# Kernel tuning notes

Hardware: AMD Instinct MI355X
Metric: run time of the kernel (lower is better)

Reference implementation:

```python
import jax, jax.numpy as jnp
import numpy as np

BLANK_IDX = -1  # resolves to V-1
BATCH_FIRST = False
IS_PROBS = False


def setup_inputs() -> dict:
    key = jax.random.key(0)
    k1, k2 = jax.random.split(key)
    T, N, V = 2048, 32, 1024
    logits = jax.random.normal(k1, (T, N, V), dtype=jnp.float32)
    in_lens = jax.random.randint(k2, (N,), 1, T + 1).astype(jnp.int64)
    return {"logits": logits, "in_lens": in_lens}


def reference(logits, in_lens):
    # logits: (T, N, V) since batch_first=False
    V = logits.shape[2]
    blank = (BLANK_IDX + V) % V  # = V - 1
    logp = jax.nn.log_softmax(logits, axis=2)
    x = jnp.transpose(logp, (1, 0, 2))  # (N, T, V)
    max_ = jnp.max(x, axis=2)            # (N, T)
    argmax = jnp.argmax(x, axis=2)       # (N, T)
    N, T = argmax.shape

    keep = argmax != blank
    dedup = jnp.concatenate(
        [keep[:, :1], keep[:, 1:] & (argmax[:, 1:] != argmax[:, :-1])], axis=1
    )
    in_len_mask = jnp.arange(T)[None, :] < in_lens[:, None]  # (N, T)
    keep = dedup & in_len_mask
    max_ = jnp.where(in_len_mask, max_, 0.0)

    out_lens = keep.sum(axis=1)  # (N,)
    # stream compaction: position of each kept token within its row
    pos = jnp.cumsum(keep, axis=1) - 1               # (N, T)
    safe_pos = jnp.where(keep, pos, T)               # out-of-bounds -> dropped
    rows = jnp.broadcast_to(jnp.arange(N)[:, None], (N, T))
    # torch masked_scatter_ semantics: overwrite first out_lens[n] slots,
    # leave remaining entries as original argmax values ("undefined" region)
    paths = argmax.at[rows, safe_pos].set(argmax, mode="drop")

    max_total = max_.sum(axis=1)  # (N,)
    if not BATCH_FIRST:
        paths = paths.T  # (T, N)
    return max_total, paths, out_lens
```

## Files before the change

### kernel.cpp

```cpp
#include <hip/hip_runtime.h>
#include <hip/hip_bf16.h>


#define WAVE 64

typedef float nvec4 __attribute__((ext_vector_type(4)));

template <int CH>
__global__ __launch_bounds__(256) void row_lse_kernel(
    const float* __restrict__ logits,
    float* __restrict__ rmaxT, int* __restrict__ rargT,
    float* __restrict__ out_paths,
    int T, int N, int rows) {
  const int lane = threadIdx.x & (WAVE - 1);
  const int w    = threadIdx.x >> 6;
  const int row  = blockIdx.x * 4 + w;
  const bool active = row < rows;
  const int V = CH * 256;
  const float* p = logits + (size_t)(active ? row : 0) * V;
  const nvec4* p4 = (const nvec4*)p;

  float m = -3.4e38f;
  int   mi = 0;
  nvec4 v[CH];
#pragma unroll
  for (int c = 0; c < CH; ++c) {
    v[c] = __builtin_nontemporal_load(p4 + c * 64 + lane);
    const int idx = c * 256 + lane * 4;
    if (v[c].x > m) { m = v[c].x; mi = idx; }
    if (v[c].y > m) { m = v[c].y; mi = idx + 1; }
    if (v[c].z > m) { m = v[c].z; mi = idx + 2; }
    if (v[c].w > m) { m = v[c].w; mi = idx + 3; }
  }
#pragma unroll
  for (int off = 32; off; off >>= 1) {
    const float om = __shfl_down(m, off);
    const int   oi = __shfl_down(mi, off);
    if (om > m || (om == m && oi < mi)) { m = om; mi = oi; }
  }
  m = __shfl(m, 0);

  float s = 0.f;
#pragma unroll
  for (int c = 0; c < CH; ++c)
    s += __expf(v[c].x - m) + __expf(v[c].y - m) +
         __expf(v[c].z - m) + __expf(v[c].w - m);
#pragma unroll
  for (int off = 32; off; off >>= 1) s += __shfl_down(s, off);

  __shared__ float s_path[4];
  if (lane == 0 && active) {
    const int t = row / N, n = row % N;
    rmaxT[(size_t)n * T + t] = -__logf(s);
    rargT[(size_t)n * T + t] = mi;
    s_path[w] = (float)mi;
  }
  __syncthreads();
  if (threadIdx.x < 4) {
    const int r = blockIdx.x * 4 + threadIdx.x;
    if (r < rows) out_paths[r] = s_path[threadIdx.x];
  }
}

__global__ __launch_bounds__(256) void row_lse_generic(
    const float* __restrict__ logits,
    float* __restrict__ rmaxT, int* __restrict__ rargT,
    float* __restrict__ out_paths,
    int T, int N, int V, int rows) {
  const int lane = threadIdx.x & (WAVE - 1);
  const int w    = threadIdx.x >> 6;
  const int row  = blockIdx.x * 4 + w;
  const bool active = row < rows;
  const float* p = logits + (size_t)(active ? row : 0) * V;

  float m = -3.4e38f; int mi = 0;
  for (int i = lane; i < V; i += WAVE) {
    const float x = p[i];
    if (x > m) { m = x; mi = i; }
  }
  for (int off = 32; off; off >>= 1) {
    const float om = __shfl_down(m, off);
    const int   oi = __shfl_down(mi, off);
    if (om > m || (om == m && oi < mi)) { m = om; mi = oi; }
  }
  m = __shfl(m, 0);
  float s = 0.f;
  for (int i = lane; i < V; i += WAVE) s += __expf(p[i] - m);
  for (int off = 32; off; off >>= 1) s += __shfl_down(s, off);

  __shared__ float s_path[4];
  if (lane == 0 && active) {
    const int t = row / N, n = row % N;
    rmaxT[(size_t)n * T + t] = -__logf(s);
    rargT[(size_t)n * T + t] = mi;
    s_path[w] = (float)mi;
  }
  __syncthreads();
  if (threadIdx.x < 4) {
    const int r = blockIdx.x * 4 + threadIdx.x;
    if (r < rows) out_paths[r] = s_path[threadIdx.x];
  }
}

#define CB 256
__global__ __launch_bounds__(CB) void ctc_compact_kernel(
    const float* __restrict__ rmaxT, const int* __restrict__ rargT,
    const int* __restrict__ in_lens, float* __restrict__ out,
    int T, int N, int V) {
  const int n = blockIdx.x;
  const int tid = threadIdx.x;
  const int L = in_lens[n];
  const int blank = V - 1;
  const int items = (T + CB - 1) / CB;
  const int t0 = tid * items;

  float* out_total = out;
  float* out_paths = out + N;
  float* out_lens  = out + N + (size_t)T * N;

  const float* rm = rmaxT + (size_t)n * T;
  const int*   ra = rargT + (size_t)n * T;

  int   cnt = 0;
  float sum = 0.f;
  int prev = (t0 > 0 && t0 <= T) ? ra[t0 - 1] : -1;
  for (int i = 0; i < items; ++i) {
    const int t = t0 + i;
    if (t >= T) break;
    const int a = ra[t];
    const bool keep = (t < L) && (a != blank) && (t == 0 || a != prev);
    prev = a;
    cnt += keep ? 1 : 0;
    if (t < L) sum += rm[t];
  }

  __shared__ int   s_cnt[CB];
  __shared__ float s_sum[CB];
  s_cnt[tid] = cnt;
  s_sum[tid] = sum;
  __syncthreads();
  for (int off = 1; off < CB; off <<= 1) {
    const int   c  = (tid >= off) ? s_cnt[tid - off] : 0;
    const float sv = (tid >= off) ? s_sum[tid - off] : 0.f;
    __syncthreads();
    s_cnt[tid] += c;
    s_sum[tid] += sv;
    __syncthreads();
  }
  const int prefix = s_cnt[tid] - cnt;
  if (tid == 0) {
    out_total[n] = s_sum[CB - 1];
    out_lens[n]  = (float)s_cnt[CB - 1];
  }

  int pos = prefix;
  prev = (t0 > 0 && t0 <= T) ? ra[t0 - 1] : -1;
  for (int i = 0; i < items; ++i) {
    const int t = t0 + i;
    if (t >= T) break;
    const int a = ra[t];
    const bool keep = (t < L) && (a != blank) && (t == 0 || a != prev);
    prev = a;
    if (keep) {
      out_paths[(size_t)pos * N + n] = (float)a;
      ++pos;
    }
  }
}

extern "C" void kernel_launch(void* const* d_in, const int* in_sizes, int n_in,
                              void* d_out, int out_size, void* d_ws, size_t ws_size,
                              hipStream_t stream) {
  const float* logits = (const float*)d_in[0];
  const int* in_lens  = (const int*)d_in[1];
  float* out = (float*)d_out;

  const int N = in_sizes[1];
  const int T = (out_size - 2 * N) / N;
  const long long total = in_sizes[0];
  const int V = (int)(total / ((long long)T * N));
  const int rows = T * N;

  float* rmaxT = (float*)d_ws;
  int*   rargT = (int*)((char*)d_ws + (size_t)rows * sizeof(float));
  float* out_paths = out + N;

  const int grid1 = (rows + 3) / 4;

  if (V == 1024) {
    row_lse_kernel<4><<<grid1, 256, 0, stream>>>(logits, rmaxT, rargT, out_paths, T, N, rows);
  } else if (V == 512) {
    row_lse_kernel<2><<<grid1, 256, 0, stream>>>(logits, rmaxT, rargT, out_paths, T, N, rows);
  } else if (V == 2048) {
    row_lse_kernel<8><<<grid1, 256, 0, stream>>>(logits, rmaxT, rargT, out_paths, T, N, rows);
  } else {
    row_lse_generic<<<grid1, 256, 0, stream>>>(logits, rmaxT, rargT, out_paths, T, N, V, rows);
  }

  ctc_compact_kernel<<<N, CB, 0, stream>>>(rmaxT, rargT, in_lens, out, T, N, V);
}
```

Baseline: 333.9 us.

## Use grid-stride row loop, drop LDS path staging, add vectorized compaction kernel

The row log-softmax kernel becomes a persistent grid-stride loop capped at 2048 blocks. It drops the shared-memory staging and barrier for path writes and swaps nontemporal loads for plain vector loads. A new compaction kernel for T=2048 loads 8 items per thread with vector loads into registers and gets the neighbour value through LDS, so it reads memory once instead of twice. The main kernel is bound by streaming the 256MB of logits, so the gain is expected to be small, and losing the nontemporal hint could change cache behaviour.

```diff
diff --git a/kernel.cpp b/kernel.cpp
--- a/kernel.cpp
+++ b/kernel.cpp
@@ -1,10 +1,10 @@
 #include <hip/hip_runtime.h>
-#include <hip/hip_bf16.h>
 
 
 #define WAVE 64
 
-typedef float nvec4 __attribute__((ext_vector_type(4)));
+typedef float fvec4 __attribute__((ext_vector_type(4)));
+typedef int   ivec4 __attribute__((ext_vector_type(4)));
 
 template <int CH>
 __global__ __launch_bounds__(256) void row_lse_kernel(
@@ -14,51 +14,46 @@
     int T, int N, int rows) {
   const int lane = threadIdx.x & (WAVE - 1);
   const int w    = threadIdx.x >> 6;
-  const int row  = blockIdx.x * 4 + w;
-  const bool active = row < rows;
   const int V = CH * 256;
-  const float* p = logits + (size_t)(active ? row : 0) * V;
-  const nvec4* p4 = (const nvec4*)p;
-
-  float m = -3.4e38f;
-  int   mi = 0;
-  nvec4 v[CH];
-#pragma unroll
-  for (int c = 0; c < CH; ++c) {
-    v[c] = __builtin_nontemporal_load(p4 + c * 64 + lane);
-    const int idx = c * 256 + lane * 4;
-    if (v[c].x > m) { m = v[c].x; mi = idx; }
-    if (v[c].y > m) { m = v[c].y; mi = idx + 1; }
-    if (v[c].z > m) { m = v[c].z; mi = idx + 2; }
-    if (v[c].w > m) { m = v[c].w; mi = idx + 3; }
-  }
-#pragma unroll
-  for (int off = 32; off; off >>= 1) {
-    const float om = __shfl_down(m, off);
-    const int   oi = __shfl_down(mi, off);
-    if (om > m || (om == m && oi < mi)) { m = om; mi = oi; }
-  }
-  m = __shfl(m, 0);
-
-  float s = 0.f;
-#pragma unroll
-  for (int c = 0; c < CH; ++c)
-    s += __expf(v[c].x - m) + __expf(v[c].y - m) +
-         __expf(v[c].z - m) + __expf(v[c].w - m);
-#pragma unroll
-  for (int off = 32; off; off >>= 1) s += __shfl_down(s, off);
-
-  __shared__ float s_path[4];
-  if (lane == 0 && active) {
-    const int t = row / N, n = row % N;
-    rmaxT[(size_t)n * T + t] = -__logf(s);
-    rargT[(size_t)n * T + t] = mi;
-    s_path[w] = (float)mi;
-  }
-  __syncthreads();
-  if (threadIdx.x < 4) {
-    const int r = blockIdx.x * 4 + threadIdx.x;
-    if (r < rows) out_paths[r] = s_path[threadIdx.x];
+  const int wstride = gridDim.x * 4;
+
+  for (int row = blockIdx.x * 4 + w; row < rows; row += wstride) {
+    const fvec4* p4 = (const fvec4*)(logits + (size_t)row * V);
+
+    float m = -3.4e38f;
+    int   mi = 0;
+    fvec4 v[CH];
+#pragma unroll
+    for (int c = 0; c < CH; ++c) {
+      v[c] = p4[c * 64 + lane];
+      const int idx = c * 256 + lane * 4;
+      if (v[c].x > m) { m = v[c].x; mi = idx; }
+      if (v[c].y > m) { m = v[c].y; mi = idx + 1; }
+      if (v[c].z > m) { m = v[c].z; mi = idx + 2; }
+      if (v[c].w > m) { m = v[c].w; mi = idx + 3; }
+    }
+#pragma unroll
+    for (int off = 32; off; off >>= 1) {
+      const float om = __shfl_down(m, off);
+      const int   oi = __shfl_down(mi, off);
+      if (om > m || (om == m && oi < mi)) { m = om; mi = oi; }
+    }
+    m = __shfl(m, 0);
+
+    float s = 0.f;
+#pragma unroll
+    for (int c = 0; c < CH; ++c)
+      s += __expf(v[c].x - m) + __expf(v[c].y - m) +
+           __expf(v[c].z - m) + __expf(v[c].w - m);
+#pragma unroll
+    for (int off = 32; off; off >>= 1) s += __shfl_down(s, off);
+
+    if (lane == 0) {
+      const int t = row / N, n = row % N;
+      rmaxT[(size_t)n * T + t] = -__logf(s);
+      rargT[(size_t)n * T + t] = mi;
+      out_paths[row] = (float)mi;
+    }
   }
 }
 
@@ -69,40 +64,108 @@
     int T, int N, int V, int rows) {
   const int lane = threadIdx.x & (WAVE - 1);
   const int w    = threadIdx.x >> 6;
-  const int row  = blockIdx.x * 4 + w;
-  const bool active = row < rows;
-  const float* p = logits + (size_t)(active ? row : 0) * V;
-
-  float m = -3.4e38f; int mi = 0;
-  for (int i = lane; i < V; i += WAVE) {
-    const float x = p[i];
-    if (x > m) { m = x; mi = i; }
-  }
-  for (int off = 32; off; off >>= 1) {
-    const float om = __shfl_down(m, off);
-    const int   oi = __shfl_down(mi, off);
-    if (om > m || (om == m && oi < mi)) { m = om; mi = oi; }
-  }
-  m = __shfl(m, 0);
-  float s = 0.f;
-  for (int i = lane; i < V; i += WAVE) s += __expf(p[i] - m);
-  for (int off = 32; off; off >>= 1) s += __shfl_down(s, off);
-
-  __shared__ float s_path[4];
-  if (lane == 0 && active) {
-    const int t = row / N, n = row % N;
-    rmaxT[(size_t)n * T + t] = -__logf(s);
-    rargT[(size_t)n * T + t] = mi;
-    s_path[w] = (float)mi;
-  }
+  const int wstride = gridDim.x * 4;
+
+  for (int row = blockIdx.x * 4 + w; row < rows; row += wstride) {
+    const float* p = logits + (size_t)row * V;
+
+    float m = -3.4e38f; int mi = 0;
+    for (int i = lane; i < V; i += WAVE) {
+      const float x = p[i];
+      if (x > m) { m = x; mi = i; }
+    }
+    for (int off = 32; off; off >>= 1) {
+      const float om = __shfl_down(m, off);
+      const int   oi = __shfl_down(mi, off);
+      if (om > m || (om == m && oi < mi)) { m = om; mi = oi; }
+    }
+    m = __shfl(m, 0);
+    float s = 0.f;
+    for (int i = lane; i < V; i += WAVE) s += __expf(p[i] - m);
+    for (int off = 32; off; off >>= 1) s += __shfl_down(s, off);
+
+    if (lane == 0) {
+      const int t = row / N, n = row % N;
+      rmaxT[(size_t)n * T + t] = -__logf(s);
+      rargT[(size_t)n * T + t] = mi;
+      out_paths[row] = (float)mi;
+    }
+  }
+}
+
+#define CB 256
+
+template <int ITEMS>
+__global__ __launch_bounds__(CB) void ctc_compact_fast(
+    const float* __restrict__ rmaxT, const int* __restrict__ rargT,
+    const int* __restrict__ in_lens, float* __restrict__ out,
+    int T, int N, int V) {
+  const int n = blockIdx.x;
+  const int tid = threadIdx.x;
+  const int L = in_lens[n];
+  const int blank = V - 1;
+  const int t0 = tid * ITEMS;
+
+  float* out_total = out;
+  float* out_paths = out + N;
+  float* out_lens  = out + N + (size_t)T * N;
+
+  const float* rm = rmaxT + (size_t)n * T;
+  const int*   ra = rargT + (size_t)n * T;
+
+  int   a[ITEMS];
+  float mv[ITEMS];
+#pragma unroll
+  for (int i = 0; i < ITEMS; i += 4) {
+    *(ivec4*)(a + i)  = *(const ivec4*)(ra + t0 + i);
+    *(fvec4*)(mv + i) = *(const fvec4*)(rm + t0 + i);
+  }
+
+  __shared__ int   s_last[CB];
+  __shared__ int   s_cnt[CB];
+  __shared__ float s_sum[CB];
+  s_last[tid] = a[ITEMS - 1];
   __syncthreads();
-  if (threadIdx.x < 4) {
-    const int r = blockIdx.x * 4 + threadIdx.x;
-    if (r < rows) out_paths[r] = s_path[threadIdx.x];
-  }
-}
-
-#define CB 256
+  int prev = (tid > 0) ? s_last[tid - 1] : -1;
+
+  bool keep[ITEMS];
+  int   cnt = 0;
+  float sum = 0.f;
+#pragma unroll
+  for (int i = 0; i < ITEMS; ++i) {
+    const int t = t0 + i;
+    keep[i] = (t < L) && (a[i] != blank) && (a[i] != prev);
+    prev = a[i];
+    cnt += keep[i] ? 1 : 0;
+    sum += (t < L) ? mv[i] : 0.f;
+  }
+
+  s_cnt[tid] = cnt;
+  s_sum[tid] = sum;
+  __syncthreads();
+  for (int off = 1; off < CB; off <<= 1) {
+    const int   c  = (tid >= off) ? s_cnt[tid - off] : 0;
+    const float sv = (tid >= off) ? s_sum[tid - off] : 0.f;
+    __syncthreads();
+    s_cnt[tid] += c;
+    s_sum[tid] += sv;
+    __syncthreads();
+  }
+  if (tid == 0) {
+    out_total[n] = s_sum[CB - 1];
+    out_lens[n]  = (float)s_cnt[CB - 1];
+  }
+
+  int pos = s_cnt[tid] - cnt;
+#pragma unroll
+  for (int i = 0; i < ITEMS; ++i) {
+    if (keep[i]) {
+      out_paths[(size_t)pos * N + n] = (float)a[i];
+      ++pos;
+    }
+  }
+}
+
 __global__ __launch_bounds__(CB) void ctc_compact_kernel(
     const float* __restrict__ rmaxT, const int* __restrict__ rargT,
     const int* __restrict__ in_lens, float* __restrict__ out,
@@ -185,7 +248,8 @@
   int*   rargT = (int*)((char*)d_ws + (size_t)rows * sizeof(float));
   float* out_paths = out + N;
 
-  const int grid1 = (rows + 3) / 4;
+  int grid1 = (rows + 3) / 4;
+  if (grid1 > 2048) grid1 = 2048;
 
   if (V == 1024) {
     row_lse_kernel<4><<<grid1, 256, 0, stream>>>(logits, rmaxT, rargT, out_paths, T, N, rows);
@@ -197,5 +261,9 @@
     row_lse_generic<<<grid1, 256, 0, stream>>>(logits, rmaxT, rargT, out_paths, T, N, V, rows);
   }
 
-  ctc_compact_kernel<<<N, CB, 0, stream>>>(rmaxT, rargT, in_lens, out, T, N, V);
-}
+  if (T == CB * 8) {
+    ctc_compact_fast<8><<<N, CB, 0, stream>>>(rmaxT, rargT, in_lens, out, T, N, V);
+  } else {
+    ctc_compact_kernel<<<N, CB, 0, stream>>>(rmaxT, rargT, in_lens, out, T, N, V);
+  }
+}
```

New measurement: 359.2 us. 7.6% more time.
